# Performance work log

Hardware: AMD Instinct MI355X
Metric: run time of the kernel (lower is better)

## Reference

```python
import jax, jax.numpy as jnp
import numpy as np
from jax import lax

D_MODEL = 384
D_STATE = 16
D_CONV = 4
EXPAND = 2
D_INNER = EXPAND * D_MODEL            # 768
DT_RANK = int(np.ceil(D_INNER / 16))  # 48
B_SZ, L_SEQ = 8, 1024
LN_EPS = 1e-5


def setup_inputs() -> dict:
    key = jax.random.key(0)
    ks = jax.random.split(key, 10)
    x = jax.random.normal(ks[0], (B_SZ, L_SEQ, D_MODEL), dtype=jnp.float32)
    ln_g = jnp.ones((D_MODEL,), jnp.float32)
    ln_b = jnp.zeros((D_MODEL,), jnp.float32)
    in_proj_w = jax.random.normal(ks[1], (2 * D_INNER, D_MODEL), jnp.float32) * (D_MODEL ** -0.5)
    conv_w = jax.random.normal(ks[2], (D_INNER, 1, D_CONV), jnp.float32) * (D_CONV ** -0.5)
    conv_b = jax.random.normal(ks[3], (D_INNER,), jnp.float32) * 0.01
    x_proj_w = jax.random.normal(ks[4], (DT_RANK + 2 * D_STATE, D_INNER), jnp.float32) * (D_INNER ** -0.5)
    dt_std = DT_RANK ** -0.5
    dt_proj_w = jax.random.uniform(ks[5], (D_INNER, DT_RANK), jnp.float32, -dt_std, dt_std)
    dt_proj_b = jax.random.normal(ks[6], (D_INNER,), jnp.float32) * 0.01
    A_log = jnp.log(jnp.tile(jnp.arange(1, D_STATE + 1, dtype=jnp.float32), (D_INNER, 1)))
    D_param = jnp.ones((D_INNER,), jnp.float32)
    out_proj_w = jax.random.normal(ks[7], (D_MODEL, D_INNER), jnp.float32) * (D_INNER ** -0.5)
    return {"x": x, "ln_g": ln_g, "ln_b": ln_b, "in_proj_w": in_proj_w,
            "conv_w": conv_w, "conv_b": conv_b, "x_proj_w": x_proj_w,
            "dt_proj_w": dt_proj_w, "dt_proj_b": dt_proj_b, "A_log": A_log,
            "D_param": D_param, "out_proj_w": out_proj_w}


def _selective_scan(u, delta, A, Bm, Cm):
    # u, delta: (B,L,Din); A: (Din,N); Bm, Cm: (B,L,N)
    dA = jnp.exp(delta[..., None] * A)                 # (B,L,Din,N)
    dBu = (delta * u)[..., None] * Bm[:, :, None, :]   # (B,L,Din,N)
    dA_t = jnp.moveaxis(dA, 1, 0)                      # (L,B,Din,N)
    dBu_t = jnp.moveaxis(dBu, 1, 0)
    C_t = jnp.moveaxis(Cm, 1, 0)                       # (L,B,N)

    def step(h, inp):
        dA_s, dBu_s, c_s = inp
        h = dA_s * h + dBu_s                           # (B,Din,N)
        y = jnp.einsum('bdn,bn->bd', h, c_s)
        return h, y

    h0 = jnp.zeros((u.shape[0], u.shape[2], A.shape[1]), u.dtype)
    _, ys = lax.scan(step, h0, (dA_t, dBu_t, C_t))
    return jnp.moveaxis(ys, 0, 1)                      # (B,L,Din)


def reference(x, ln_g, ln_b, in_proj_w, conv_w, conv_b, x_proj_w,
              dt_proj_w, dt_proj_b, A_log, D_param, out_proj_w):
    residual = x
    # LayerNorm
    mu = jnp.mean(x, axis=-1, keepdims=True)
    var = jnp.var(x, axis=-1, keepdims=True)
    xn = (x - mu) * lax.rsqrt(var + LN_EPS) * ln_g + ln_b
    # in_proj and split
    xz = xn @ in_proj_w.T                              # (B,L,2*Din)
    xh, z = jnp.split(xz, 2, axis=-1)
    # causal depthwise conv1d (torch pads both sides then truncates to L)
    xc = lax.conv_general_dilated(
        jnp.moveaxis(xh, 1, 2), conv_w, (1,), [(D_CONV - 1, 0)],
        feature_group_count=D_INNER,
        dimension_numbers=('NCH', 'OIH', 'NCH')) + conv_b[None, :, None]
    u = jax.nn.silu(jnp.moveaxis(xc, 1, 2))            # (B,L,Din)
    # SSM input-dependent params
    xpo = u @ x_proj_w.T                               # (B,L,dt_rank+2N)
    dlow, Bm, Cm = jnp.split(xpo, [DT_RANK, DT_RANK + D_STATE], axis=-1)
    delta = jax.nn.softplus(dlow @ dt_proj_w.T + dt_proj_b)
    A = -jnp.exp(A_log)
    y = _selective_scan(u, delta, A, Bm, Cm)
    y = y + u * D_param
    y = y * jax.nn.silu(z)
    out = y @ out_proj_w.T
    return residual + out
```

## Files before the change

kernel.cpp:

```cpp
#include <hip/hip_runtime.h>
#include <math.h>

#define DMODEL 384
#define DIN 768
#define NST 16
#define DTR 48
#define BSZ 8
#define LSEQ 1024
#define NROWS (BSZ*LSEQ)
#define XPO_W (DTR + 2*NST)
#define CL 32
#define NC (LSEQ/CL)
#define CSEG 32

typedef __attribute__((ext_vector_type(8))) short bf16x8;
typedef __attribute__((ext_vector_type(4))) float f32x4;

__device__ __forceinline__ unsigned short f2bf(float x) {
  unsigned int u = __float_as_uint(x);
  unsigned int r = u + 0x7fffu + ((u >> 16) & 1u);
  return (unsigned short)(r >> 16);
}
__device__ __forceinline__ float bf2f(unsigned short h) {
  return __uint_as_float(((unsigned int)h) << 16);
}
__device__ __forceinline__ unsigned int pk2(float a, float b) {
  return (unsigned int)f2bf(a) | ((unsigned int)f2bf(b) << 16);
}

__device__ __forceinline__ void gll16(const void* g, void* l) {
  __builtin_amdgcn_global_load_lds(
      (const __attribute__((address_space(1))) void*)g,
      (__attribute__((address_space(3))) void*)l, 16, 0, 0);
}

__global__ __launch_bounds__(256) void ln_kernel(const float* __restrict__ x,
    const float* __restrict__ g, const float* __restrict__ b,
    unsigned short* __restrict__ xh, unsigned short* __restrict__ xl) {
  int row = blockIdx.x * 4 + (threadIdx.x >> 6);
  int lane = threadIdx.x & 63;
  const float* xr = x + (size_t)row * DMODEL;
  float v[6];
  float s = 0.f, ss = 0.f;
#pragma unroll
  for (int i = 0; i < 6; ++i) { v[i] = xr[lane + i*64]; s += v[i]; ss += v[i]*v[i]; }
#pragma unroll
  for (int off = 32; off; off >>= 1) { s += __shfl_xor(s, off); ss += __shfl_xor(ss, off); }
  float mu = s * (1.f / DMODEL);
  float var = ss * (1.f / DMODEL) - mu * mu;
  float inv = rsqrtf(var + 1e-5f);
#pragma unroll
  for (int i = 0; i < 6; ++i) {
    int c = lane + i*64;
    float o = (v[i] - mu) * inv * g[c] + b[c];
    unsigned short hv = f2bf(o);
    xh[(size_t)row*DMODEL + c] = hv;
    xl[(size_t)row*DMODEL + c] = f2bf(o - bf2f(hv));
  }
}

__device__ __forceinline__ void split_one(const float* src, int ldsrc, int R, int C,
    unsigned short* dh, unsigned short* dl, int Cpad, int i) {
  int r = i / Cpad, c = i - r * Cpad;
  float v = (r < R && c < C) ? src[(size_t)r*ldsrc + c] : 0.f;
  unsigned short hv = f2bf(v);
  dh[i] = hv;
  dl[i] = f2bf(v - bf2f(hv));
}
#define N_INW (1536*384)
#define N_XW  (128*768)
#define N_DTW (768*64)
#define N_OW  (384*768)
__global__ __launch_bounds__(256) void split_weights(
    const float* __restrict__ inw, const float* __restrict__ xw,
    const float* __restrict__ dtw, const float* __restrict__ ow,
    unsigned short* inw_h, unsigned short* inw_l,
    unsigned short* xw_h, unsigned short* xw_l,
    unsigned short* dtw_h, unsigned short* dtw_l,
    unsigned short* ow_h, unsigned short* ow_l) {
  int i = blockIdx.x * 256 + threadIdx.x;
  if (i < N_INW) { split_one(inw, 384, 1536, 384, inw_h, inw_l, 384, i); return; }
  i -= N_INW;
  if (i < N_XW)  { split_one(xw, 768, 80, 768, xw_h, xw_l, 768, i); return; }
  i -= N_XW;
  if (i < N_DTW) { split_one(dtw, 48, 768, 48, dtw_h, dtw_l, 64, i); return; }
  i -= N_DTW;
  if (i < N_OW)  { split_one(ow, 768, 384, 768, ow_h, ow_l, 768, i); return; }
}

template<int EPI>
__global__ __launch_bounds__(256, 2) void gemm_mfma(
    const unsigned short* __restrict__ Ah, const unsigned short* __restrict__ Al, int lda,
    const unsigned short* __restrict__ Bh, const unsigned short* __restrict__ Bl, int ldb,
    float* __restrict__ C, int ldc, size_t strideS,
    const float* __restrict__ bias, const float* __restrict__ res,
    int T) {
  __shared__ unsigned short lds[2][4][4096];
  int tid = threadIdx.x;
  int lane = tid & 63, wid = tid >> 6;
  int wm = wid >> 1, wn = wid & 1;

  unsigned nwg = gridDim.x * gridDim.y;
  unsigned bid = blockIdx.y * gridDim.x + blockIdx.x;
  unsigned cpx = nwg >> 3;
  unsigned sw = (bid & 7) * cpx + (bid >> 3);
  unsigned bx = sw % gridDim.x, by = sw / gridDim.x;
  int m0 = by * 128, n0 = bx * 128;
  C += (size_t)blockIdx.z * strideS;
  size_t kofs = (size_t)blockIdx.z * T * 32;

  f32x4 acc[4][4];
#pragma unroll
  for (int i = 0; i < 4; ++i)
#pragma unroll
    for (int j = 0; j < 4; ++j) acc[i][j] = (f32x4){0.f, 0.f, 0.f, 0.f};

  int kgl = lane >> 4, rl = lane & 15;

  int c0 = wid*128 + lane;
  int c1 = wid*128 + 64 + lane;
  int r0 = c0 & 127, kg0 = c0 >> 7;
  int r1 = c1 & 127, kg1 = c1 >> 7;

#define STAGE(bf, kt) do { \
    size_t ga0 = (size_t)(m0 + r0) * lda + (kt) + kg0*8 + kofs; \
    size_t gb0 = (size_t)(n0 + r0) * ldb + (kt) + kg0*8 + kofs; \
    size_t ga1 = (size_t)(m0 + r1) * lda + (kt) + kg1*8 + kofs; \
    size_t gb1 = (size_t)(n0 + r1) * ldb + (kt) + kg1*8 + kofs; \
    gll16(Ah + ga0, &lds[bf][0][(wid*128)*8]); \
    gll16(Al + ga0, &lds[bf][1][(wid*128)*8]); \
    gll16(Bh + gb0, &lds[bf][2][(wid*128)*8]); \
    gll16(Bl + gb0, &lds[bf][3][(wid*128)*8]); \
    gll16(Ah + ga1, &lds[bf][0][(wid*128+64)*8]); \
    gll16(Al + ga1, &lds[bf][1][(wid*128+64)*8]); \
    gll16(Bh + gb1, &lds[bf][2][(wid*128+64)*8]); \
    gll16(Bl + gb1, &lds[bf][3][(wid*128+64)*8]); \
  } while (0)

  STAGE(0, 0);
  asm volatile("s_waitcnt vmcnt(0)" ::: "memory");
  __builtin_amdgcn_s_barrier();

  int cur = 0;
  for (int t = 0; t < T; ++t) {
    if (t + 1 < T) {
      STAGE(cur ^ 1, (t + 1) << 5);
    }
    asm volatile("" ::: "memory");
    bf16x8 ah[4], al[4], bh[4], bl[4];
#pragma unroll
    for (int mi = 0; mi < 4; ++mi) {
      int cell = kgl*128 + wm*64 + mi*16 + rl;
      ah[mi] = *reinterpret_cast<const bf16x8*>(&lds[cur][0][cell*8]);
      al[mi] = *reinterpret_cast<const bf16x8*>(&lds[cur][1][cell*8]);
    }
#pragma unroll
    for (int ni = 0; ni < 4; ++ni) {
      int cell = kgl*128 + wn*64 + ni*16 + rl;
      bh[ni] = *reinterpret_cast<const bf16x8*>(&lds[cur][2][cell*8]);
      bl[ni] = *reinterpret_cast<const bf16x8*>(&lds[cur][3][cell*8]);
    }
#pragma unroll
    for (int mi = 0; mi < 4; ++mi)
#pragma unroll
      for (int ni = 0; ni < 4; ++ni) {
        acc[mi][ni] = __builtin_amdgcn_mfma_f32_16x16x32_bf16(ah[mi], bh[ni], acc[mi][ni], 0, 0, 0);
        acc[mi][ni] = __builtin_amdgcn_mfma_f32_16x16x32_bf16(al[mi], bh[ni], acc[mi][ni], 0, 0, 0);
        acc[mi][ni] = __builtin_amdgcn_mfma_f32_16x16x32_bf16(ah[mi], bl[ni], acc[mi][ni], 0, 0, 0);
      }
    asm volatile("s_waitcnt vmcnt(0)" ::: "memory");
    __builtin_amdgcn_s_barrier();
    cur ^= 1;
  }
#undef STAGE

#pragma unroll
  for (int mi = 0; mi < 4; ++mi)
#pragma unroll
    for (int ni = 0; ni < 4; ++ni)
#pragma unroll
      for (int j = 0; j < 4; ++j) {
        int m = m0 + wm*64 + mi*16 + (lane>>4)*4 + j;
        int n = n0 + wn*64 + ni*16 + (lane&15);
        float v = acc[mi][ni][j];
        if (EPI == 0) {
          C[(size_t)m*ldc + n] = v;
        } else if (EPI == 2) {
          v += bias[n];
          v = (v > 20.f) ? v : log1pf(__expf(v));
          C[(size_t)m*ldc + n] = v;
        } else if (EPI == 3) {
          C[(size_t)m*ldc + n] = v + res[(size_t)m*ldc + n];
        }
      }
}

__global__ __launch_bounds__(256) void reduce_xproj(
    const float* __restrict__ P, float* __restrict__ xpo,
    unsigned short* __restrict__ dh, unsigned short* __restrict__ dl) {
  int idx = blockIdx.x * 256 + threadIdx.x;
  int m = idx >> 7, n = idx & 127;
  float v = 0.f;
#pragma unroll
  for (int s = 0; s < 4; ++s) v += P[(size_t)s * NROWS * 128 + idx];
  if (n < XPO_W) xpo[(size_t)m * XPO_W + n] = v;
  if (n < 64) {
    unsigned short hv = f2bf(v);
    dh[(size_t)m*64 + n] = hv;
    dl[(size_t)m*64 + n] = f2bf(v - bf2f(hv));
  }
}

__global__ __launch_bounds__(256) void reduce_out(
    const float* __restrict__ P, const float* __restrict__ x, float* __restrict__ out) {
  int i = blockIdx.x * 256 + threadIdx.x;
  const size_t S = (size_t)NROWS*DMODEL;
  out[i] = x[i] + ((P[i] + P[i + S]) + (P[i + 2*S] + P[i + 3*S]));
}

__global__ __launch_bounds__(256) void conv_silu_kernel(
    const float* __restrict__ xz, const float* __restrict__ w,
    const float* __restrict__ cb,
    unsigned short* __restrict__ uh, unsigned short* __restrict__ ul) {
  int d = blockIdx.x * 256 + threadIdx.x;
  int l0 = blockIdx.y * CSEG;
  int b = blockIdx.z;
  float xv[CSEG + 3];
#pragma unroll
  for (int i = 0; i < CSEG + 3; ++i) {
    int l = l0 + i - 3;
    xv[i] = (l >= 0) ? xz[((size_t)b*LSEQ + l) * (2*DIN) + d] : 0.f;
  }
  float w0 = w[d*4], w1 = w[d*4+1], w2 = w[d*4+2], w3 = w[d*4+3];
  float cbv = cb[d];
#pragma unroll
  for (int i = 0; i < CSEG; ++i) {
    float acc = cbv;
    acc = fmaf(xv[i],     w0, acc);
    acc = fmaf(xv[i + 1], w1, acc);
    acc = fmaf(xv[i + 2], w2, acc);
    acc = fmaf(xv[i + 3], w3, acc);
    float s = acc / (1.f + __expf(-acc));
    size_t idx = ((size_t)b*LSEQ + l0 + i) * DIN + d;
    unsigned short hv = f2bf(s);
    uh[idx] = hv;
    ul[idx] = f2bf(s - bf2f(hv));
  }
}

__global__ __launch_bounds__(256) void scan_pass1(
    const float* __restrict__ delta,
    const unsigned short* __restrict__ uh, const unsigned short* __restrict__ ul,
    const float* __restrict__ xpo, const float* __restrict__ A_log,
    unsigned short* __restrict__ carryA, unsigned short* __restrict__ carryH) {
  int d = blockIdx.x * 256 + threadIdx.x;
  int c = blockIdx.y, b = blockIdx.z;
  float A[16];
  {
    const float4* al = reinterpret_cast<const float4*>(A_log + (size_t)d * NST);
#pragma unroll
    for (int i = 0; i < 4; ++i) {
      float4 t = al[i];
      A[4*i+0] = -__expf(t.x); A[4*i+1] = -__expf(t.y);
      A[4*i+2] = -__expf(t.z); A[4*i+3] = -__expf(t.w);
    }
  }
  float h[16], ap[16];
#pragma unroll
  for (int n = 0; n < 16; ++n) { h[n] = 0.f; ap[n] = 1.f; }
  const float* dp = delta + ((size_t)b*LSEQ + c*CL) * DIN + d;
  const unsigned short* uhp = uh + ((size_t)b*LSEQ + c*CL) * DIN + d;
  const unsigned short* ulp = ul + ((size_t)b*LSEQ + c*CL) * DIN + d;
  const float* bp = xpo   + ((size_t)b*LSEQ + c*CL) * XPO_W + DTR;
  for (int l = 0; l < CL; ++l) {
    float dv = dp[(size_t)l*DIN];
    float uv = bf2f(uhp[(size_t)l*DIN]) + bf2f(ulp[(size_t)l*DIN]);
    float du = dv * uv;
    float Bv[16];
    {
      const float4* b4 = reinterpret_cast<const float4*>(bp + (size_t)l*XPO_W);
#pragma unroll
      for (int i = 0; i < 4; ++i) {
        float4 t = b4[i];
        Bv[4*i+0] = t.x; Bv[4*i+1] = t.y; Bv[4*i+2] = t.z; Bv[4*i+3] = t.w;
      }
    }
#pragma unroll
    for (int n = 0; n < 16; ++n) {
      float a = __expf(dv * A[n]);
      ap[n] *= a;
      h[n] = fmaf(a, h[n], du * Bv[n]);
    }
  }
  size_t ci = (((size_t)b*NC + c) * DIN + d) * NST;
  uint4* ca = reinterpret_cast<uint4*>(carryA + ci);
  uint4* ch = reinterpret_cast<uint4*>(carryH + ci);
  ca[0] = make_uint4(pk2(ap[0],ap[1]), pk2(ap[2],ap[3]), pk2(ap[4],ap[5]), pk2(ap[6],ap[7]));
  ca[1] = make_uint4(pk2(ap[8],ap[9]), pk2(ap[10],ap[11]), pk2(ap[12],ap[13]), pk2(ap[14],ap[15]));
  ch[0] = make_uint4(pk2(h[0],h[1]), pk2(h[2],h[3]), pk2(h[4],h[5]), pk2(h[6],h[7]));
  ch[1] = make_uint4(pk2(h[8],h[9]), pk2(h[10],h[11]), pk2(h[12],h[13]), pk2(h[14],h[15]));
}

__global__ __launch_bounds__(256) void scan_mid(
    const unsigned short* __restrict__ carryA, unsigned short* __restrict__ carryH) {
  int idx = blockIdx.x * 256 + threadIdx.x;
  int b = idx / (DIN*NST);
  int rem = idx - b * DIN*NST;
  float h = 0.f;
#pragma unroll
  for (int c = 0; c < NC; ++c) {
    size_t i = ((size_t)b*NC + c) * (DIN*NST) + rem;
    float a = bf2f(carryA[i]);
    float e = bf2f(carryH[i]);
    carryH[i] = f2bf(h);
    h = fmaf(a, h, e);
  }
}

__global__ __launch_bounds__(256) void scan_pass2(
    const float* __restrict__ delta,
    const unsigned short* __restrict__ uh, const unsigned short* __restrict__ ul,
    const float* __restrict__ xpo, const float* __restrict__ xz,
    const float* __restrict__ A_log, const float* __restrict__ Dp,
    const unsigned short* __restrict__ carryH,
    unsigned short* __restrict__ yh, unsigned short* __restrict__ yl) {
  int d = blockIdx.x * 256 + threadIdx.x;
  int c = blockIdx.y, b = blockIdx.z;
  float A[16];
  {
    const float4* al = reinterpret_cast<const float4*>(A_log + (size_t)d * NST);
#pragma unroll
    for (int i = 0; i < 4; ++i) {
      float4 t = al[i];
      A[4*i+0] = -__expf(t.x); A[4*i+1] = -__expf(t.y);
      A[4*i+2] = -__expf(t.z); A[4*i+3] = -__expf(t.w);
    }
  }
  float h[16];
  size_t ci = (((size_t)b*NC + c) * DIN + d) * NST;
  {
    const uint4* ch4 = reinterpret_cast<const uint4*>(carryH + ci);
    uint4 t0 = ch4[0], t1 = ch4[1];
    h[0] = bf2f(t0.x & 0xffff); h[1] = bf2f(t0.x >> 16);
    h[2] = bf2f(t0.y & 0xffff); h[3] = bf2f(t0.y >> 16);
    h[4] = bf2f(t0.z & 0xffff); h[5] = bf2f(t0.z >> 16);
    h[6] = bf2f(t0.w & 0xffff); h[7] = bf2f(t0.w >> 16);
    h[8] = bf2f(t1.x & 0xffff); h[9] = bf2f(t1.x >> 16);
    h[10] = bf2f(t1.y & 0xffff); h[11] = bf2f(t1.y >> 16);
    h[12] = bf2f(t1.z & 0xffff); h[13] = bf2f(t1.z >> 16);
    h[14] = bf2f(t1.w & 0xffff); h[15] = bf2f(t1.w >> 16);
  }
  float Dd = Dp[d];
  const float* dp = delta + ((size_t)b*LSEQ + c*CL) * DIN + d;
  const unsigned short* uhp = uh + ((size_t)b*LSEQ + c*CL) * DIN + d;
  const unsigned short* ulp = ul + ((size_t)b*LSEQ + c*CL) * DIN + d;
  const float* bp = xpo   + ((size_t)b*LSEQ + c*CL) * XPO_W + DTR;
  const float* zp = xz    + ((size_t)b*LSEQ + c*CL) * (2*DIN) + DIN + d;
  size_t yi0 = ((size_t)b*LSEQ + c*CL) * DIN + d;
  for (int l = 0; l < CL; ++l) {
    float dv = dp[(size_t)l*DIN];
    float uv = bf2f(uhp[(size_t)l*DIN]) + bf2f(ulp[(size_t)l*DIN]);
    float du = dv * uv;
    float Bv[16], Cv[16];
    {
      const float4* b4 = reinterpret_cast<const float4*>(bp + (size_t)l*XPO_W);
#pragma unroll
      for (int i = 0; i < 4; ++i) {
        float4 t = b4[i];
        Bv[4*i+0] = t.x; Bv[4*i+1] = t.y; Bv[4*i+2] = t.z; Bv[4*i+3] = t.w;
        float4 tc = b4[i+4];
        Cv[4*i+0] = tc.x; Cv[4*i+1] = tc.y; Cv[4*i+2] = tc.z; Cv[4*i+3] = tc.w;
      }
    }
    float p = 0.f;
#pragma unroll
    for (int n = 0; n < 16; ++n) {
      float a = __expf(dv * A[n]);
      h[n] = fmaf(a, h[n], du * Bv[n]);
      p = fmaf(h[n], Cv[n], p);
    }
    float z = zp[(size_t)l*(2*DIN)];
    float sz = z / (1.f + __expf(-z));
    float yv = fmaf(uv, Dd, p) * sz;
    unsigned short hv = f2bf(yv);
    yh[yi0 + (size_t)l*DIN] = hv;
    yl[yi0 + (size_t)l*DIN] = f2bf(yv - bf2f(hv));
  }
}

extern "C" void kernel_launch(void* const* d_in, const int* in_sizes, int n_in,
                              void* d_out, int out_size, void* d_ws, size_t ws_size,
                              hipStream_t stream) {
  const float* x          = (const float*)d_in[0];
  const float* ln_g       = (const float*)d_in[1];
  const float* ln_b       = (const float*)d_in[2];
  const float* in_proj_w  = (const float*)d_in[3];
  const float* conv_w     = (const float*)d_in[4];
  const float* conv_b     = (const float*)d_in[5];
  const float* x_proj_w   = (const float*)d_in[6];
  const float* dt_proj_w  = (const float*)d_in[7];
  const float* dt_proj_b  = (const float*)d_in[8];
  const float* A_log      = (const float*)d_in[9];
  const float* D_param    = (const float*)d_in[10];
  const float* out_proj_w = (const float*)d_in[11];

  char* w = (char*)d_ws;
  unsigned short* xn_h  = (unsigned short*)w;
  unsigned short* xn_l  = xn_h + (size_t)NROWS*DMODEL;
  unsigned short* dlow_h = (unsigned short*)w;
  unsigned short* dlow_l = dlow_h + (size_t)NROWS*64;
  unsigned short* carryA = (unsigned short*)w;
  unsigned short* carryH = carryA + (size_t)BSZ*NC*DIN*NST;
  char* p = w + (size_t)NROWS*DMODEL*4;
  float* xz = (float*)p;              p += (size_t)NROWS*2*DIN*4;
  unsigned short* u_h = (unsigned short*)p;
  unsigned short* u_l = u_h + (size_t)NROWS*DIN;      p += (size_t)NROWS*DIN*4;
  float* xpo = (float*)p;             p += (size_t)NROWS*XPO_W*4;
  float* delta = (float*)p;           p += (size_t)NROWS*DIN*4;
  unsigned short* inw_h = (unsigned short*)delta;
  unsigned short* inw_l = inw_h + (size_t)1536*384;
  unsigned short* xw_h  = inw_l + (size_t)1536*384;
  unsigned short* xw_l  = xw_h + (size_t)128*768;
  unsigned short* y2_h = (unsigned short*)p;
  unsigned short* y2_l = y2_h + (size_t)NROWS*DIN;
  float* xpart = (float*)p;           p += (size_t)NROWS*DIN*4;
  unsigned short* dtw_h = (unsigned short*)p;
  unsigned short* dtw_l = dtw_h + (size_t)768*64;
  unsigned short* ow_h  = dtw_l + (size_t)768*64;
  unsigned short* ow_l  = ow_h + (size_t)384*768;
  float* opart = xz;

  split_weights<<<(N_INW+N_XW+N_DTW+N_OW)/256, 256, 0, stream>>>(
      in_proj_w, x_proj_w, dt_proj_w, out_proj_w,
      inw_h, inw_l, xw_h, xw_l, dtw_h, dtw_l, ow_h, ow_l);

  ln_kernel<<<NROWS/4, 256, 0, stream>>>(x, ln_g, ln_b, xn_h, xn_l);

  gemm_mfma<0><<<dim3(12, 64, 1), 256, 0, stream>>>(xn_h, xn_l, DMODEL, inw_h, inw_l, DMODEL,
      xz, 2*DIN, 0, nullptr, nullptr, 12);

  conv_silu_kernel<<<dim3(DIN/256, LSEQ/CSEG, BSZ), 256, 0, stream>>>(
      xz, conv_w, conv_b, u_h, u_l);

  gemm_mfma<0><<<dim3(1, 64, 4), 256, 0, stream>>>(u_h, u_l, DIN, xw_h, xw_l, DIN,
      xpart, 128, (size_t)NROWS*128, nullptr, nullptr, 6);
  reduce_xproj<<<(NROWS*128)/256, 256, 0, stream>>>(xpart, xpo, dlow_h, dlow_l);

  gemm_mfma<2><<<dim3(6, 64, 1), 256, 0, stream>>>(dlow_h, dlow_l, 64, dtw_h, dtw_l, 64,
      delta, DIN, 0, dt_proj_b, nullptr, 2);

  {
    dim3 g1(DIN/256, NC, BSZ);
    scan_pass1<<<g1, 256, 0, stream>>>(delta, u_h, u_l, xpo, A_log, carryA, carryH);
    scan_mid<<<(BSZ*DIN*NST)/256, 256, 0, stream>>>(carryA, carryH);
    scan_pass2<<<g1, 256, 0, stream>>>(delta, u_h, u_l, xpo, xz, A_log, D_param,
                                       carryH, y2_h, y2_l);
  }

  gemm_mfma<0><<<dim3(3, 64, 4), 256, 0, stream>>>(y2_h, y2_l, DIN, ow_h, ow_l, DIN,
      opart, DMODEL, (size_t)NROWS*DMODEL, nullptr, nullptr, 6);
  reduce_out<<<(NROWS*DMODEL)/256, 256, 0, stream>>>(opart, x, (float*)d_out);
}
```

Before: 229.9 us.

## Fuse LN into weight prep, precompute silu(z) in in_proj epilogue, drop u low bits

```diff
diff --git a/kernel.cpp b/kernel.cpp
--- a/kernel.cpp
+++ b/kernel.cpp
@@ -34,31 +34,6 @@
       (__attribute__((address_space(3))) void*)l, 16, 0, 0);
 }
 
-__global__ __launch_bounds__(256) void ln_kernel(const float* __restrict__ x,
-    const float* __restrict__ g, const float* __restrict__ b,
-    unsigned short* __restrict__ xh, unsigned short* __restrict__ xl) {
-  int row = blockIdx.x * 4 + (threadIdx.x >> 6);
-  int lane = threadIdx.x & 63;
-  const float* xr = x + (size_t)row * DMODEL;
-  float v[6];
-  float s = 0.f, ss = 0.f;
-#pragma unroll
-  for (int i = 0; i < 6; ++i) { v[i] = xr[lane + i*64]; s += v[i]; ss += v[i]*v[i]; }
-#pragma unroll
-  for (int off = 32; off; off >>= 1) { s += __shfl_xor(s, off); ss += __shfl_xor(ss, off); }
-  float mu = s * (1.f / DMODEL);
-  float var = ss * (1.f / DMODEL) - mu * mu;
-  float inv = rsqrtf(var + 1e-5f);
-#pragma unroll
-  for (int i = 0; i < 6; ++i) {
-    int c = lane + i*64;
-    float o = (v[i] - mu) * inv * g[c] + b[c];
-    unsigned short hv = f2bf(o);
-    xh[(size_t)row*DMODEL + c] = hv;
-    xl[(size_t)row*DMODEL + c] = f2bf(o - bf2f(hv));
-  }
-}
-
 __device__ __forceinline__ void split_one(const float* src, int ldsrc, int R, int C,
     unsigned short* dh, unsigned short* dl, int Cpad, int i) {
   int r = i / Cpad, c = i - r * Cpad;
@@ -71,21 +46,48 @@
 #define N_XW  (128*768)
 #define N_DTW (768*64)
 #define N_OW  (384*768)
-__global__ __launch_bounds__(256) void split_weights(
+#define NWBLK ((N_INW+N_XW+N_DTW+N_OW)/256)
+__global__ __launch_bounds__(256) void prep_kernel(
     const float* __restrict__ inw, const float* __restrict__ xw,
     const float* __restrict__ dtw, const float* __restrict__ ow,
     unsigned short* inw_h, unsigned short* inw_l,
     unsigned short* xw_h, unsigned short* xw_l,
     unsigned short* dtw_h, unsigned short* dtw_l,
-    unsigned short* ow_h, unsigned short* ow_l) {
-  int i = blockIdx.x * 256 + threadIdx.x;
-  if (i < N_INW) { split_one(inw, 384, 1536, 384, inw_h, inw_l, 384, i); return; }
-  i -= N_INW;
-  if (i < N_XW)  { split_one(xw, 768, 80, 768, xw_h, xw_l, 768, i); return; }
-  i -= N_XW;
-  if (i < N_DTW) { split_one(dtw, 48, 768, 48, dtw_h, dtw_l, 64, i); return; }
-  i -= N_DTW;
-  if (i < N_OW)  { split_one(ow, 768, 384, 768, ow_h, ow_l, 768, i); return; }
+    unsigned short* ow_h, unsigned short* ow_l,
+    const float* __restrict__ x, const float* __restrict__ g,
+    const float* __restrict__ b,
+    unsigned short* __restrict__ xh, unsigned short* __restrict__ xl) {
+  if (blockIdx.x < NWBLK) {
+    int i = blockIdx.x * 256 + threadIdx.x;
+    if (i < N_INW) { split_one(inw, 384, 1536, 384, inw_h, inw_l, 384, i); return; }
+    i -= N_INW;
+    if (i < N_XW)  { split_one(xw, 768, 80, 768, xw_h, xw_l, 768, i); return; }
+    i -= N_XW;
+    if (i < N_DTW) { split_one(dtw, 48, 768, 48, dtw_h, dtw_l, 64, i); return; }
+    i -= N_DTW;
+    split_one(ow, 768, 384, 768, ow_h, ow_l, 768, i);
+    return;
+  }
+  int row = (blockIdx.x - NWBLK) * 4 + (threadIdx.x >> 6);
+  int lane = threadIdx.x & 63;
+  const float* xr = x + (size_t)row * DMODEL;
+  float v[6];
+  float s = 0.f, ss = 0.f;
+#pragma unroll
+  for (int i = 0; i < 6; ++i) { v[i] = xr[lane + i*64]; s += v[i]; ss += v[i]*v[i]; }
+#pragma unroll
+  for (int off = 32; off; off >>= 1) { s += __shfl_xor(s, off); ss += __shfl_xor(ss, off); }
+  float mu = s * (1.f / DMODEL);
+  float var = ss * (1.f / DMODEL) - mu * mu;
+  float inv = rsqrtf(var + 1e-5f);
+#pragma unroll
+  for (int i = 0; i < 6; ++i) {
+    int c = lane + i*64;
+    float o = (v[i] - mu) * inv * g[c] + b[c];
+    unsigned short hv = f2bf(o);
+    xh[(size_t)row*DMODEL + c] = hv;
+    xl[(size_t)row*DMODEL + c] = f2bf(o - bf2f(hv));
+  }
 }
 
 template<int EPI>
@@ -93,7 +95,7 @@
     const unsigned short* __restrict__ Ah, const unsigned short* __restrict__ Al, int lda,
     const unsigned short* __restrict__ Bh, const unsigned short* __restrict__ Bl, int ldb,
     float* __restrict__ C, int ldc, size_t strideS,
-    const float* __restrict__ bias, const float* __restrict__ res,
+    const float* __restrict__ bias, unsigned short* __restrict__ sz,
     int T) {
   __shared__ unsigned short lds[2][4][4096];
   int tid = threadIdx.x;
@@ -189,8 +191,13 @@
           v += bias[n];
           v = (v > 20.f) ? v : log1pf(__expf(v));
           C[(size_t)m*ldc + n] = v;
-        } else if (EPI == 3) {
-          C[(size_t)m*ldc + n] = v + res[(size_t)m*ldc + n];
+        } else if (EPI == 5) {
+          if (n < DIN) {
+            C[(size_t)m*DIN + n] = v;
+          } else {
+            float s = v / (1.f + __expf(-v));
+            sz[(size_t)m*DIN + (n - DIN)] = f2bf(s);
+          }
         }
       }
 }
@@ -202,7 +209,7 @@
   int m = idx >> 7, n = idx & 127;
   float v = 0.f;
 #pragma unroll
-  for (int s = 0; s < 4; ++s) v += P[(size_t)s * NROWS * 128 + idx];
+  for (int s = 0; s < 6; ++s) v += P[(size_t)s * NROWS * 128 + idx];
   if (n < XPO_W) xpo[(size_t)m * XPO_W + n] = v;
   if (n < 64) {
     unsigned short hv = f2bf(v);
@@ -219,7 +226,7 @@
 }
 
 __global__ __launch_bounds__(256) void conv_silu_kernel(
-    const float* __restrict__ xz, const float* __restrict__ w,
+    const float* __restrict__ xh32, const float* __restrict__ w,
     const float* __restrict__ cb,
     unsigned short* __restrict__ uh, unsigned short* __restrict__ ul) {
   int d = blockIdx.x * 256 + threadIdx.x;
@@ -229,7 +236,7 @@
 #pragma unroll
   for (int i = 0; i < CSEG + 3; ++i) {
     int l = l0 + i - 3;
-    xv[i] = (l >= 0) ? xz[((size_t)b*LSEQ + l) * (2*DIN) + d] : 0.f;
+    xv[i] = (l >= 0) ? xh32[((size_t)b*LSEQ + l) * DIN + d] : 0.f;
   }
   float w0 = w[d*4], w1 = w[d*4+1], w2 = w[d*4+2], w3 = w[d*4+3];
   float cbv = cb[d];
@@ -250,7 +257,7 @@
 
 __global__ __launch_bounds__(256) void scan_pass1(
     const float* __restrict__ delta,
-    const unsigned short* __restrict__ uh, const unsigned short* __restrict__ ul,
+    const unsigned short* __restrict__ uh,
     const float* __restrict__ xpo, const float* __restrict__ A_log,
     unsigned short* __restrict__ carryA, unsigned short* __restrict__ carryH) {
   int d = blockIdx.x * 256 + threadIdx.x;
@@ -270,11 +277,10 @@
   for (int n = 0; n < 16; ++n) { h[n] = 0.f; ap[n] = 1.f; }
   const float* dp = delta + ((size_t)b*LSEQ + c*CL) * DIN + d;
   const unsigned short* uhp = uh + ((size_t)b*LSEQ + c*CL) * DIN + d;
-  const unsigned short* ulp = ul + ((size_t)b*LSEQ + c*CL) * DIN + d;
   const float* bp = xpo   + ((size_t)b*LSEQ + c*CL) * XPO_W + DTR;
   for (int l = 0; l < CL; ++l) {
     float dv = dp[(size_t)l*DIN];
-    float uv = bf2f(uhp[(size_t)l*DIN]) + bf2f(ulp[(size_t)l*DIN]);
+    float uv = bf2f(uhp[(size_t)l*DIN]);
     float du = dv * uv;
     float Bv[16];
     {
@@ -319,8 +325,8 @@
 
 __global__ __launch_bounds__(256) void scan_pass2(
     const float* __restrict__ delta,
-    const unsigned short* __restrict__ uh, const unsigned short* __restrict__ ul,
-    const float* __restrict__ xpo, const float* __restrict__ xz,
+    const unsigned short* __restrict__ uh,
+    const float* __restrict__ xpo, const unsigned short* __restrict__ sz,
     const float* __restrict__ A_log, const float* __restrict__ Dp,
     const unsigned short* __restrict__ carryH,
     unsigned short* __restrict__ yh, unsigned short* __restrict__ yl) {
@@ -353,13 +359,12 @@
   float Dd = Dp[d];
   const float* dp = delta + ((size_t)b*LSEQ + c*CL) * DIN + d;
   const unsigned short* uhp = uh + ((size_t)b*LSEQ + c*CL) * DIN + d;
-  const unsigned short* ulp = ul + ((size_t)b*LSEQ + c*CL) * DIN + d;
   const float* bp = xpo   + ((size_t)b*LSEQ + c*CL) * XPO_W + DTR;
-  const float* zp = xz    + ((size_t)b*LSEQ + c*CL) * (2*DIN) + DIN + d;
+  const unsigned short* szp = sz + ((size_t)b*LSEQ + c*CL) * DIN + d;
   size_t yi0 = ((size_t)b*LSEQ + c*CL) * DIN + d;
   for (int l = 0; l < CL; ++l) {
     float dv = dp[(size_t)l*DIN];
-    float uv = bf2f(uhp[(size_t)l*DIN]) + bf2f(ulp[(size_t)l*DIN]);
+    float uv = bf2f(uhp[(size_t)l*DIN]);
     float du = dv * uv;
     float Bv[16], Cv[16];
     {
@@ -379,9 +384,8 @@
       h[n] = fmaf(a, h[n], du * Bv[n]);
       p = fmaf(h[n], Cv[n], p);
     }
-    float z = zp[(size_t)l*(2*DIN)];
-    float sz = z / (1.f + __expf(-z));
-    float yv = fmaf(uv, Dd, p) * sz;
+    float sv = bf2f(szp[(size_t)l*DIN]);
+    float yv = fmaf(uv, Dd, p) * sv;
     unsigned short hv = f2bf(yv);
     yh[yi0 + (size_t)l*DIN] = hv;
     yl[yi0 + (size_t)l*DIN] = f2bf(yv - bf2f(hv));
@@ -412,7 +416,9 @@
   unsigned short* carryA = (unsigned short*)w;
   unsigned short* carryH = carryA + (size_t)BSZ*NC*DIN*NST;
   char* p = w + (size_t)NROWS*DMODEL*4;
-  float* xz = (float*)p;              p += (size_t)NROWS*2*DIN*4;
+  float* xh32 = (float*)p;
+  unsigned short* sz = (unsigned short*)(p + (size_t)NROWS*DIN*4);
+  float* opart = (float*)p;           p += (size_t)NROWS*2*DIN*4;
   unsigned short* u_h = (unsigned short*)p;
   unsigned short* u_l = u_h + (size_t)NROWS*DIN;      p += (size_t)NROWS*DIN*4;
   float* xpo = (float*)p;             p += (size_t)NROWS*XPO_W*4;
@@ -428,22 +434,20 @@
   unsigned short* dtw_l = dtw_h + (size_t)768*64;
   unsigned short* ow_h  = dtw_l + (size_t)768*64;
   unsigned short* ow_l  = ow_h + (size_t)384*768;
-  float* opart = xz;
-
-  split_weights<<<(N_INW+N_XW+N_DTW+N_OW)/256, 256, 0, stream>>>(
+
+  prep_kernel<<<NWBLK + NROWS/4, 256, 0, stream>>>(
       in_proj_w, x_proj_w, dt_proj_w, out_proj_w,
-      inw_h, inw_l, xw_h, xw_l, dtw_h, dtw_l, ow_h, ow_l);
-
-  ln_kernel<<<NROWS/4, 256, 0, stream>>>(x, ln_g, ln_b, xn_h, xn_l);
-
-  gemm_mfma<0><<<dim3(12, 64, 1), 256, 0, stream>>>(xn_h, xn_l, DMODEL, inw_h, inw_l, DMODEL,
-      xz, 2*DIN, 0, nullptr, nullptr, 12);
+      inw_h, inw_l, xw_h, xw_l, dtw_h, dtw_l, ow_h, ow_l,
+      x, ln_g, ln_b, xn_h, xn_l);
+
+  gemm_mfma<5><<<dim3(12, 64, 1), 256, 0, stream>>>(xn_h, xn_l, DMODEL, inw_h, inw_l, DMODEL,
+      xh32, DIN, 0, nullptr, sz, 12);
 
   conv_silu_kernel<<<dim3(DIN/256, LSEQ/CSEG, BSZ), 256, 0, stream>>>(
-      xz, conv_w, conv_b, u_h, u_l);
-
-  gemm_mfma<0><<<dim3(1, 64, 4), 256, 0, stream>>>(u_h, u_l, DIN, xw_h, xw_l, DIN,
-      xpart, 128, (size_t)NROWS*128, nullptr, nullptr, 6);
+      xh32, conv_w, conv_b, u_h, u_l);
+
+  gemm_mfma<0><<<dim3(1, 64, 6), 256, 0, stream>>>(u_h, u_l, DIN, xw_h, xw_l, DIN,
+      xpart, 128, (size_t)NROWS*128, nullptr, nullptr, 4);
   reduce_xproj<<<(NROWS*128)/256, 256, 0, stream>>>(xpart, xpo, dlow_h, dlow_l);
 
   gemm_mfma<2><<<dim3(6, 64, 1), 256, 0, stream>>>(dlow_h, dlow_l, 64, dtw_h, dtw_l, 64,
@@ -451,9 +455,9 @@
 
   {
     dim3 g1(DIN/256, NC, BSZ);
-    scan_pass1<<<g1, 256, 0, stream>>>(delta, u_h, u_l, xpo, A_log, carryA, carryH);
+    scan_pass1<<<g1, 256, 0, stream>>>(delta, u_h, xpo, A_log, carryA, carryH);
     scan_mid<<<(BSZ*DIN*NST)/256, 256, 0, stream>>>(carryA, carryH);
-    scan_pass2<<<g1, 256, 0, stream>>>(delta, u_h, u_l, xpo, xz, A_log, D_param,
+    scan_pass2<<<g1, 256, 0, stream>>>(delta, u_h, xpo, sz, A_log, D_param,
                                        carryH, y2_h, y2_l);
   }
 
```

New measurement: 241.6 us. +5.1%, slower.
